# Kernel tuning notes

Hardware: AMD Instinct MI355X
Metric: run time of the kernel (lower is better)

The kernel has to match this reference:

```python
import jax, jax.numpy as jnp
import numpy as np

EPS = 1e-6  # flax nnx LayerNorm default

def _ln(x):
    # LayerNorm without scale/bias
    m = jnp.mean(x, axis=-1, keepdims=True)
    v = jnp.mean(jnp.square(x - m), axis=-1, keepdims=True)
    return (x - m) * jax.lax.rsqrt(v + EPS)

def _modulate(x, shift, scale):
    return x * (1.0 + scale[:, None]) + shift[:, None]

def setup_inputs() -> dict:
    key = jax.random.key(0)
    B, S, H, NH = 8, 1024, 1024, 16
    ks = jax.random.split(key, 12)
    s = lambda k, sh: jax.random.normal(k, sh, dtype=jnp.float32) * 0.02
    return {
        "x": jax.random.normal(ks[0], (B, S, H), dtype=jnp.float32),
        "c": jax.random.normal(ks[1], (B, H), dtype=jnp.float32),
        "w_ada": s(ks[2], (H, 6 * H)),
        "b_ada": jnp.zeros((6 * H,), dtype=jnp.float32),
        "w_qkv": s(ks[3], (H, 3 * H)),
        "w_proj": s(ks[4], (H, H)),
        "b_proj": jnp.zeros((H,), dtype=jnp.float32),
        "w_mlp1": s(ks[5], (H, 4 * H)),
        "b_mlp1": jnp.zeros((4 * H,), dtype=jnp.float32),
        "w_mlp2": s(ks[6], (4 * H, H)),
        "b_mlp2": jnp.zeros((H,), dtype=jnp.float32),
    }

def reference(x, c, w_ada, b_ada, w_qkv, w_proj, b_proj, w_mlp1, b_mlp1, w_mlp2, b_mlp2):
    B, S, H = x.shape
    NH = 16
    CH = H // NH
    # adaLN modulation: silu -> Linear
    cmod = jax.nn.silu(c) @ w_ada + b_ada  # [B, 6H]
    shift_msa, scale_msa, gate_msa, shift_mlp, scale_mlp, gate_mlp = jnp.split(cmod, 6, axis=-1)
    # attention branch
    x_mod = _modulate(_ln(x), shift_msa, scale_msa)
    qkv = x_mod @ w_qkv  # [B, S, 3H]
    k, q, v = jnp.split(qkv, 3, axis=-1)  # note source order: k, q, v
    k = k.reshape(B, S, NH, CH)
    q = q.reshape(B, S, NH, CH)
    v = v.reshape(B, S, NH, CH)
    q = q / CH  # faithful: divide by head_dim (not sqrt)
    w = jnp.einsum('bqhc,bkhc->bhqk', q, k).astype(jnp.float32)
    w = jax.nn.softmax(w, axis=-1)
    y = jnp.einsum('bhqk,bkhc->bqhc', w, v).reshape(B, S, H)
    attn_x = y @ w_proj + b_proj
    x = x + gate_msa[:, None] * attn_x
    # MLP branch
    x_mod2 = _modulate(_ln(x), shift_mlp, scale_mlp)
    h = jax.nn.gelu(x_mod2 @ w_mlp1 + b_mlp1)
    mlp_x = h @ w_mlp2 + b_mlp2
    x = x + gate_mlp[:, None] * mlp_x
    return x
```

## Files before the change

### kernel.cpp

```cpp
#include <hip/hip_runtime.h>
#include <stdint.h>

typedef unsigned short u16;
using bf16x8 = __attribute__((ext_vector_type(8))) __bf16;
using f32x4  = __attribute__((ext_vector_type(4))) float;

#define MFMA16(a,b,c) __builtin_amdgcn_mfma_f32_16x16x32_bf16((a),(b),(c),0,0,0)

__device__ __forceinline__ u16 f2bf(float f) {
  union { float f; uint32_t u; } v; v.f = f;
  uint32_t r = v.u + 0x7FFFu + ((v.u >> 16) & 1u);
  return (u16)(r >> 16);
}

__device__ __forceinline__ void gload_lds16(const void* g, void* l) {
  typedef const __attribute__((address_space(1))) void* gp_t;
  typedef __attribute__((address_space(3))) void* lp_t;
  __builtin_amdgcn_global_load_lds((gp_t)(uintptr_t)g,
                                   (lp_t)(uint32_t)(uintptr_t)l, 16, 0, 0);
}

__global__ __launch_bounds__(256)
void adaln_part_k(const float* __restrict__ c, const float* __restrict__ w,
                  float* __restrict__ partial) {
  const int jb = blockIdx.x, ks = blockIdx.y;
  const int j = jb * 256 + threadIdx.x;
  __shared__ float sil[8][32];
  {
    int b = threadIdx.x >> 5, kk = threadIdx.x & 31;
    float v = c[b * 1024 + ks * 32 + kk];
    sil[b][kk] = v / (1.f + __expf(-v));
  }
  __syncthreads();
  float acc[8] = {0,0,0,0,0,0,0,0};
#pragma unroll 8
  for (int kk = 0; kk < 32; ++kk) {
    float wv = w[(size_t)(ks * 32 + kk) * 6144 + j];
#pragma unroll
    for (int b = 0; b < 8; ++b) acc[b] += sil[b][kk] * wv;
  }
#pragma unroll
  for (int b = 0; b < 8; ++b)
    partial[((size_t)ks * 8 + b) * 6144 + j] = acc[b];
}

__global__ __launch_bounds__(256)
void adaln_red_k(const float* __restrict__ partial, const float* __restrict__ bias,
                 float* __restrict__ cmod) {
  int g = blockIdx.x * 256 + threadIdx.x;
  int j = g % 6144;
  float s = bias[j];
#pragma unroll 8
  for (int ks = 0; ks < 32; ++ks)
    s += partial[(size_t)ks * 8 * 6144 + g];
  cmod[g] = s;
}

__global__ __launch_bounds__(256)
void tcast_k(const float* __restrict__ in, u16* __restrict__ out, int K, int N,
             int lo, int hi, float scale) {
  __shared__ u16 t[64][65];
  int n0 = blockIdx.x * 64, k0 = blockIdx.y * 64;
#pragma unroll
  for (int i = 0; i < 16; ++i) {
    int idx = i * 256 + threadIdx.x;
    int r = idx >> 6, cc = idx & 63;
    float v = in[(size_t)(k0 + r) * N + n0 + cc];
    int n = n0 + cc;
    if (n >= lo && n < hi) v *= scale;
    t[r][cc] = f2bf(v);
  }
  __syncthreads();
#pragma unroll
  for (int i = 0; i < 16; ++i) {
    int idx = i * 256 + threadIdx.x;
    int r = idx >> 6, cc = idx & 63;
    out[(size_t)(n0 + r) * K + k0 + cc] = t[cc][r];
  }
}

__global__ __launch_bounds__(256)
void lnmod_k(const float* __restrict__ x, const float* __restrict__ cmod,
             int shift_off, int scale_off, u16* __restrict__ out) {
  int row = blockIdx.x;
  int b = row >> 10;
  const float4* xr = (const float4*)(x + (size_t)row * 1024);
  float4 v = xr[threadIdx.x];
  float s = v.x + v.y + v.z + v.w;
  float sq = v.x * v.x + v.y * v.y + v.z * v.z + v.w * v.w;
#pragma unroll
  for (int m = 32; m >= 1; m >>= 1) {
    s  += __shfl_xor(s, m);
    sq += __shfl_xor(sq, m);
  }
  __shared__ float ss[4], ssq[4];
  int wave = threadIdx.x >> 6, lane = threadIdx.x & 63;
  if (lane == 0) { ss[wave] = s; ssq[wave] = sq; }
  __syncthreads();
  s  = ss[0] + ss[1] + ss[2] + ss[3];
  sq = ssq[0] + ssq[1] + ssq[2] + ssq[3];
  float mean = s * (1.f / 1024.f);
  float var  = sq * (1.f / 1024.f) - mean * mean;
  float rstd = rsqrtf(var + 1e-6f);
  int col = threadIdx.x * 4;
  const float* sh = cmod + (size_t)b * 6144 + shift_off + col;
  const float* sc = cmod + (size_t)b * 6144 + scale_off + col;
  float xv[4] = {v.x, v.y, v.z, v.w};
  union { u16 o[4]; uint64_t u; } pk;
#pragma unroll
  for (int j = 0; j < 4; ++j)
    pk.o[j] = f2bf((xv[j] - mean) * rstd * (1.f + sc[j]) + sh[j]);
  *(uint64_t*)(out + (size_t)row * 1024 + col) = pk.u;
}

__global__ __launch_bounds__(256)
void tv_k(const u16* __restrict__ qkv, u16* __restrict__ vt) {
  __shared__ u16 t[64][65];
  int r0 = blockIdx.x * 64;
  int h = blockIdx.y;
  int b = r0 >> 10;
  int s0 = r0 & 1023;
#pragma unroll
  for (int i = 0; i < 16; ++i) {
    int idx = i * 256 + threadIdx.x;
    int r = idx >> 6, cc = idx & 63;
    t[r][cc] = qkv[(size_t)(r0 + r) * 3072 + 2048 + h * 64 + cc];
  }
  __syncthreads();
#pragma unroll
  for (int i = 0; i < 16; ++i) {
    int idx = i * 256 + threadIdx.x;
    int ch = idx >> 6, scc = idx & 63;
    vt[((size_t)(b * 16 + h) * 64 + ch) * 1024 + s0 + scc] = t[scc][ch];
  }
}

__device__ __forceinline__ float gelu_f(float x) {
  float z = 1.5957691216057308f * (x + 0.044715f * x * x * x);
  return x / (1.f + __expf(-z));
}

template <int EP>
__global__ __launch_bounds__(512, 2)
void gemm_k(const u16* __restrict__ A, const u16* __restrict__ Bt,
            int N, int K,
            const float* __restrict__ bias, const float* __restrict__ resid,
            const float* __restrict__ gate, void* __restrict__ outp) {
  __shared__ __align__(16) u16 Asb[3][256 * 64];
  __shared__ __align__(16) u16 Bsb[3][128 * 64];
  const int bn = blockIdx.x, bm = blockIdx.y;
  const int tid = threadIdx.x;
  const int wave = tid >> 6, lane = tid & 63;
  const int l15 = lane & 15, lhi = lane >> 4;
  const int wr = wave >> 1, wc = wave & 1;
  const int nkt = K >> 6;
  const size_t arow0 = (size_t)bm * 256;
  const size_t brow0 = (size_t)bn * 128;

  f32x4 acc[4][4] = {};

  auto stage = [&](int buf, int kt) {
    const u16* ab = A  + arow0 * K + (size_t)kt * 64;
    const u16* bb = Bt + brow0 * K + (size_t)kt * 64;
#pragma unroll
    for (int i = 0; i < 4; ++i) {
      int q = i * 512 + tid;
      int r = q >> 3, c = (q & 7) ^ (r & 7);
      gload_lds16(ab + (size_t)r * K + c * 8, &Asb[buf][(i * 8 + wave) * 512]);
    }
#pragma unroll
    for (int i = 0; i < 2; ++i) {
      int q = i * 512 + tid;
      int r = q >> 3, c = (q & 7) ^ (r & 7);
      gload_lds16(bb + (size_t)r * K + c * 8, &Bsb[buf][(i * 8 + wave) * 512]);
    }
  };

  stage(0, 0);
  if (nkt > 1) stage(1, 1);
  asm volatile("s_waitcnt vmcnt(6)" ::: "memory");
  __syncthreads();

  for (int t = 0; t < nkt; ++t) {
    const int s = t % 3;
    if (t + 2 < nkt) stage((t + 2) % 3, t + 2);

    bf16x8 af[4][2], bfr[4][2];
#pragma unroll
    for (int m = 0; m < 4; ++m) {
      int r = wr * 64 + m * 16 + l15;
#pragma unroll
      for (int kh = 0; kh < 2; ++kh) {
        int c = (kh * 4 + lhi) ^ (r & 7);
        af[m][kh] = *(const bf16x8*)&Asb[s][r * 64 + c * 8];
      }
    }
#pragma unroll
    for (int n = 0; n < 4; ++n) {
      int r = wc * 64 + n * 16 + l15;
#pragma unroll
      for (int kh = 0; kh < 2; ++kh) {
        int c = (kh * 4 + lhi) ^ (r & 7);
        bfr[n][kh] = *(const bf16x8*)&Bsb[s][r * 64 + c * 8];
      }
    }
    __builtin_amdgcn_s_setprio(1);
#pragma unroll
    for (int kh = 0; kh < 2; ++kh)
#pragma unroll
      for (int m = 0; m < 4; ++m)
#pragma unroll
        for (int n = 0; n < 4; ++n)
          acc[m][n] = MFMA16(af[m][kh], bfr[n][kh], acc[m][n]);
    __builtin_amdgcn_s_setprio(0);

    if (t + 1 < nkt) {
      if (t + 2 < nkt) asm volatile("s_waitcnt vmcnt(6)" ::: "memory");
      else             asm volatile("s_waitcnt vmcnt(0)" ::: "memory");
      __syncthreads();
    }
  }

#pragma unroll
  for (int m = 0; m < 4; ++m) {
    int row = bm * 256 + wr * 64 + m * 16 + lhi * 4;
#pragma unroll
    for (int n = 0; n < 4; ++n) {
      int col = bn * 128 + wc * 64 + n * 16 + l15;
#pragma unroll
      for (int r = 0; r < 4; ++r) {
        int rr = row + r;
        float v = acc[m][n][r];
        if (EP == 0) {
          ((u16*)outp)[(size_t)rr * N + col] = f2bf(v);
        } else if (EP == 1) {
          ((u16*)outp)[(size_t)rr * N + col] = f2bf(gelu_f(v + bias[col]));
        } else {
          float t2 = v + bias[col];
          int b = rr >> 10;
          float res = resid[(size_t)rr * N + col];
          ((float*)outp)[(size_t)rr * N + col] = res + gate[(size_t)b * 6144 + col] * t2;
        }
      }
    }
  }
}

__global__ __launch_bounds__(256)
void attn_k(const u16* __restrict__ qkv, const u16* __restrict__ vt,
            u16* __restrict__ y) {
  const int qt = blockIdx.x, h = blockIdx.y, b = blockIdx.z;
  const int tid = threadIdx.x, wave = tid >> 6, lane = tid & 63;
  const int l15 = lane & 15, lhi = lane >> 4;
  __shared__ __align__(16) u16 Qs[64 * 64];
  __shared__ __align__(16) u16 Ks[2][64 * 64];
  __shared__ __align__(16) u16 Vs[2][64 * 64];
  __shared__ __align__(16) u16 Ps[64 * 64];
  const size_t qrow0 = (size_t)b * 1024 + qt * 64;
  const size_t krow0 = (size_t)b * 1024;
  const size_t vrow0 = (size_t)(b * 16 + h) * 64;

  auto stageQ = [&]() {
#pragma unroll
    for (int i = 0; i < 2; ++i) {
      int c = (i * 4 + wave) * 64 + lane;
      int r = c >> 3, j = (c & 7) ^ (c >> 3 & 7);
      gload_lds16(qkv + (qrow0 + r) * 3072 + 1024 + h * 64 + j * 8,
                  &Qs[(i * 4 + wave) * 512]);
    }
  };
  auto stageKV = [&](int buf, int kt) {
#pragma unroll
    for (int i = 0; i < 2; ++i) {
      int c = (i * 4 + wave) * 64 + lane;
      int r = c >> 3, j = (c & 7) ^ (c >> 3 & 7);
      gload_lds16(qkv + (krow0 + kt * 64 + r) * 3072 + h * 64 + j * 8,
                  &Ks[buf][(i * 4 + wave) * 512]);
      gload_lds16(vt + (vrow0 + r) * 1024 + kt * 64 + j * 8,
                  &Vs[buf][(i * 4 + wave) * 512]);
    }
  };
  auto ldb = [](const u16* base, int row, int cc) -> bf16x8 {
    return *(const bf16x8*)&base[row * 64 + ((cc ^ (row & 7)) << 3)];
  };

  stageQ();
  stageKV(0, 0);
  __syncthreads();
  bf16x8 qf[2];
  qf[0] = ldb(Qs, wave * 16 + l15, lhi);
  qf[1] = ldb(Qs, wave * 16 + l15, 4 + lhi);

  bf16x8 ones;
#pragma unroll
  for (int j = 0; j < 8; ++j) ones[j] = (__bf16)1.0f;

  float m_r[4];
  f32x4 o[5] = {};
#pragma unroll
  for (int r = 0; r < 4; ++r) m_r[r] = -3.0e38f;

  for (int kt = 0; kt < 16; ++kt) {
    int cur = kt & 1;
    if (kt < 15) stageKV(cur ^ 1, kt + 1);
    f32x4 sf[4] = {};
    __builtin_amdgcn_s_setprio(1);
#pragma unroll
    for (int n = 0; n < 4; ++n) {
      bf16x8 k0 = ldb(Ks[cur], n * 16 + l15, lhi);
      bf16x8 k1 = ldb(Ks[cur], n * 16 + l15, 4 + lhi);
      sf[n] = MFMA16(qf[0], k0, sf[n]);
      sf[n] = MFMA16(qf[1], k1, sf[n]);
    }
    __builtin_amdgcn_s_setprio(0);
#pragma unroll
    for (int r = 0; r < 4; ++r) {
      float mx = fmaxf(fmaxf(sf[0][r], sf[1][r]), fmaxf(sf[2][r], sf[3][r]));
      mx = fmaxf(mx, __shfl_xor(mx, 1));
      mx = fmaxf(mx, __shfl_xor(mx, 2));
      mx = fmaxf(mx, __shfl_xor(mx, 4));
      mx = fmaxf(mx, __shfl_xor(mx, 8));
      float mn = fmaxf(m_r[r], mx);
      float al = __expf(m_r[r] - mn);
      m_r[r] = mn;
      float p0 = __expf(sf[0][r] - mn);
      float p1 = __expf(sf[1][r] - mn);
      float p2 = __expf(sf[2][r] - mn);
      float p3 = __expf(sf[3][r] - mn);
      o[0][r] *= al; o[1][r] *= al; o[2][r] *= al; o[3][r] *= al; o[4][r] *= al;
      int row = wave * 16 + lhi * 4 + r;
      int rb = row * 64, sw = (row & 7) << 3;
      Ps[rb + (l15 ^ sw)]        = f2bf(p0);
      Ps[rb + ((l15 + 16) ^ sw)] = f2bf(p1);
      Ps[rb + ((l15 + 32) ^ sw)] = f2bf(p2);
      Ps[rb + ((l15 + 48) ^ sw)] = f2bf(p3);
    }
    bf16x8 pf0 = ldb(Ps, wave * 16 + l15, lhi);
    bf16x8 pf1 = ldb(Ps, wave * 16 + l15, 4 + lhi);
    __builtin_amdgcn_s_setprio(1);
#pragma unroll
    for (int n = 0; n < 4; ++n) {
      bf16x8 v0 = ldb(Vs[cur], n * 16 + l15, lhi);
      bf16x8 v1 = ldb(Vs[cur], n * 16 + l15, 4 + lhi);
      o[n] = MFMA16(pf0, v0, o[n]);
      o[n] = MFMA16(pf1, v1, o[n]);
    }
    o[4] = MFMA16(pf0, ones, o[4]);
    o[4] = MFMA16(pf1, ones, o[4]);
    __builtin_amdgcn_s_setprio(0);
    __syncthreads();
  }
#pragma unroll
  for (int r = 0; r < 4; ++r) {
    float inv = 1.0f / o[4][r];
    size_t yrow = (qrow0 + wave * 16 + lhi * 4 + r) * 1024 + h * 64 + l15;
    y[yrow]      = f2bf(o[0][r] * inv);
    y[yrow + 16] = f2bf(o[1][r] * inv);
    y[yrow + 32] = f2bf(o[2][r] * inv);
    y[yrow + 48] = f2bf(o[3][r] * inv);
  }
}

extern "C" void kernel_launch(void* const* d_in, const int* in_sizes, int n_in,
                              void* d_out, int out_size, void* d_ws, size_t ws_size,
                              hipStream_t stream) {
  const float* x      = (const float*)d_in[0];
  const float* c      = (const float*)d_in[1];
  const float* w_ada  = (const float*)d_in[2];
  const float* b_ada  = (const float*)d_in[3];
  const float* w_qkv  = (const float*)d_in[4];
  const float* w_proj = (const float*)d_in[5];
  const float* b_proj = (const float*)d_in[6];
  const float* w_mlp1 = (const float*)d_in[7];
  const float* b_mlp1 = (const float*)d_in[8];
  const float* w_mlp2 = (const float*)d_in[9];
  const float* b_mlp2 = (const float*)d_in[10];
  float* out = (float*)d_out;

  char* ws = (char*)d_ws;
  size_t off = 0;
  auto alloc = [&](size_t bytes) {
    void* p = ws + off;
    off += (bytes + 255) & ~(size_t)255;
    return p;
  };
  float* cmod  = (float*)alloc((size_t)8 * 6144 * 4);
  float* apart = (float*)alloc((size_t)32 * 8 * 6144 * 4);
  u16* wqkvT   = (u16*)alloc((size_t)3072 * 1024 * 2);
  u16* wprojT  = (u16*)alloc((size_t)1024 * 1024 * 2);
  u16* wmlp1T  = (u16*)alloc((size_t)4096 * 1024 * 2);
  u16* wmlp2T  = (u16*)alloc((size_t)1024 * 4096 * 2);
  u16* xmod    = (u16*)alloc((size_t)8192 * 1024 * 2);
  u16* qkv     = (u16*)alloc((size_t)8192 * 3072 * 2);
  u16* vt      = (u16*)alloc((size_t)8 * 16 * 64 * 1024 * 2);
  float* x1    = (float*)alloc((size_t)8192 * 1024 * 4);
  u16* hbuf    = (u16*)alloc((size_t)8192 * 4096 * 2);
  u16* ybuf  = xmod;
  u16* xmod2 = qkv;

  adaln_part_k<<<dim3(24, 32), 256, 0, stream>>>(c, w_ada, apart);
  adaln_red_k<<<192, 256, 0, stream>>>(apart, b_ada, cmod);
  tcast_k<<<dim3(3072 / 64, 1024 / 64), 256, 0, stream>>>(w_qkv,  wqkvT,  1024, 3072,
                                                          1024, 2048, 1.0f / 64.0f);
  tcast_k<<<dim3(1024 / 64, 1024 / 64), 256, 0, stream>>>(w_proj, wprojT, 1024, 1024, 0, 0, 1.f);
  tcast_k<<<dim3(4096 / 64, 1024 / 64), 256, 0, stream>>>(w_mlp1, wmlp1T, 1024, 4096, 0, 0, 1.f);
  tcast_k<<<dim3(1024 / 64, 4096 / 64), 256, 0, stream>>>(w_mlp2, wmlp2T, 4096, 1024, 0, 0, 1.f);
  lnmod_k<<<8192, 256, 0, stream>>>(x, cmod, 0, 1024, xmod);
  gemm_k<0><<<dim3(3072 / 128, 8192 / 256), 512, 0, stream>>>(
      xmod, wqkvT, 3072, 1024, nullptr, nullptr, nullptr, qkv);
  tv_k<<<dim3(128, 16), 256, 0, stream>>>(qkv, vt);
  attn_k<<<dim3(16, 16, 8), 256, 0, stream>>>(qkv, vt, ybuf);
  gemm_k<2><<<dim3(1024 / 128, 8192 / 256), 512, 0, stream>>>(
      ybuf, wprojT, 1024, 1024, b_proj, x, cmod + 2048, x1);
  lnmod_k<<<8192, 256, 0, stream>>>(x1, cmod, 3072, 4096, xmod2);
  gemm_k<1><<<dim3(4096 / 128, 8192 / 256), 512, 0, stream>>>(
      xmod2, wmlp1T, 4096, 1024, b_mlp1, nullptr, nullptr, hbuf);
  gemm_k<2><<<dim3(1024 / 128, 8192 / 256), 512, 0, stream>>>(
      hbuf, wmlp2T, 1024, 4096, b_mlp2, x1, cmod + 5120, out);
}
```

Measured before the change: 417.3 us.

## Restructure GEMM into 8-wave ping-pong schedule with interleaved prefetch and barriers

The GEMM kernel changes its wave layout from 4x2 to 2x4 and gives each wave two 64-row halves of A against two 16-column B fragments. Each K-step is split into four MFMA phases separated by s_barrier and sched_barrier, and the next tile's global-to-LDS loads are issued in thirds between the phases. The aim is to overlap LDS fragment loads and global prefetch with MFMA work and keep waves in lockstep. The cost is many more barriers per K-step and a different LDS read pattern, which may stall if phases are unbalanced.

```diff
diff --git a/kernel.cpp b/kernel.cpp
--- a/kernel.cpp
+++ b/kernel.cpp
@@ -6,6 +6,7 @@
 using f32x4  = __attribute__((ext_vector_type(4))) float;
 
 #define MFMA16(a,b,c) __builtin_amdgcn_mfma_f32_16x16x32_bf16((a),(b),(c),0,0,0)
+#define SB0() __builtin_amdgcn_sched_barrier(0)
 
 __device__ __forceinline__ u16 f2bf(float f) {
   union { float f; uint32_t u; } v; v.f = f;
@@ -142,104 +143,144 @@
 
 template <int EP>
 __global__ __launch_bounds__(512, 2)
-void gemm_k(const u16* __restrict__ A, const u16* __restrict__ Bt,
-            int N, int K,
-            const float* __restrict__ bias, const float* __restrict__ resid,
-            const float* __restrict__ gate, void* __restrict__ outp) {
-  __shared__ __align__(16) u16 Asb[3][256 * 64];
-  __shared__ __align__(16) u16 Bsb[3][128 * 64];
+void gemm8_k(const u16* __restrict__ A, const u16* __restrict__ Bt,
+             int N, int K,
+             const float* __restrict__ bias, const float* __restrict__ resid,
+             const float* __restrict__ gate, void* __restrict__ outp) {
+  __shared__ __align__(16) u16 As[3][256 * 64];
+  __shared__ __align__(16) u16 Bs[3][128 * 64];
   const int bn = blockIdx.x, bm = blockIdx.y;
   const int tid = threadIdx.x;
   const int wave = tid >> 6, lane = tid & 63;
   const int l15 = lane & 15, lhi = lane >> 4;
-  const int wr = wave >> 1, wc = wave & 1;
+  const int wm = wave >> 2, wn = wave & 3;
   const int nkt = K >> 6;
   const size_t arow0 = (size_t)bm * 256;
   const size_t brow0 = (size_t)bn * 128;
 
-  f32x4 acc[4][4] = {};
-
-  auto stage = [&](int buf, int kt) {
-    const u16* ab = A  + arow0 * K + (size_t)kt * 64;
-    const u16* bb = Bt + brow0 * K + (size_t)kt * 64;
-#pragma unroll
-    for (int i = 0; i < 4; ++i) {
-      int q = i * 512 + tid;
-      int r = q >> 3, c = (q & 7) ^ (r & 7);
-      gload_lds16(ab + (size_t)r * K + c * 8, &Asb[buf][(i * 8 + wave) * 512]);
-    }
-#pragma unroll
-    for (int i = 0; i < 2; ++i) {
-      int q = i * 512 + tid;
-      int r = q >> 3, c = (q & 7) ^ (r & 7);
-      gload_lds16(bb + (size_t)r * K + c * 8, &Bsb[buf][(i * 8 + wave) * 512]);
-    }
-  };
-
-  stage(0, 0);
-  if (nkt > 1) stage(1, 1);
-  asm volatile("s_waitcnt vmcnt(6)" ::: "memory");
-  __syncthreads();
-
-  for (int t = 0; t < nkt; ++t) {
-    const int s = t % 3;
-    if (t + 2 < nkt) stage((t + 2) % 3, t + 2);
-
-    bf16x8 af[4][2], bfr[4][2];
+  f32x4 acc[2][4][2] = {};
+
+  auto stage_half = [&](int half, int w, int kt) {
+    if (half < 2) {
+      const u16* ab = A + (arow0 + half * 128) * (size_t)K + (size_t)kt * 64;
+#pragma unroll
+      for (int i = 0; i < 2; ++i) {
+        int q = i * 512 + tid;
+        int r = q >> 3, cc = (q & 7) ^ (r & 7);
+        gload_lds16(ab + (size_t)r * K + cc * 8,
+                    &As[w][(half * 16 + i * 8 + wave) * 512]);
+      }
+    } else {
+      const u16* bb = Bt + brow0 * (size_t)K + (size_t)kt * 64;
+#pragma unroll
+      for (int i = 0; i < 2; ++i) {
+        int q = i * 512 + tid;
+        int r = q >> 3, cc = (q & 7) ^ (r & 7);
+        gload_lds16(bb + (size_t)r * K + cc * 8,
+                    &Bs[w][(i * 8 + wave) * 512]);
+      }
+    }
+  };
+  auto lda = [&](int s, int mh, int m, int kk) -> bf16x8 {
+    int r = wm * 128 + mh * 64 + m * 16 + l15;
+    int cc = (kk * 4 + lhi) ^ (r & 7);
+    return *(const bf16x8*)&As[s][r * 64 + cc * 8];
+  };
+  auto ldbf = [&](int s, int nh, int kk) -> bf16x8 {
+    int r = wn * 32 + nh * 16 + l15;
+    int cc = (kk * 4 + lhi) ^ (r & 7);
+    return *(const bf16x8*)&Bs[s][r * 64 + cc * 8];
+  };
+
+  stage_half(0, 0, 0); stage_half(1, 0, 0); stage_half(2, 0, 0);
+  if (nkt > 1) {
+    stage_half(0, 1, 1); stage_half(1, 1, 1); stage_half(2, 1, 1);
+    asm volatile("s_waitcnt vmcnt(6)" ::: "memory");
+  } else {
+    asm volatile("s_waitcnt vmcnt(0)" ::: "memory");
+  }
+  SB0(); __builtin_amdgcn_s_barrier(); SB0();
+
+  for (int kt = 0; kt < nkt; ++kt) {
+    const int s = kt % 3, w2 = (kt + 2) % 3;
+    const bool pf = (kt + 2 < nkt);
+    bf16x8 afr[4][2], bfr[2][2];
+
+#pragma unroll
+    for (int m = 0; m < 4; ++m) { afr[m][0] = lda(s, 0, m, 0); afr[m][1] = lda(s, 0, m, 1); }
+    bfr[0][0] = ldbf(s, 0, 0); bfr[0][1] = ldbf(s, 0, 1);
+    if (pf) stage_half(0, w2, kt + 2);
+    SB0(); __builtin_amdgcn_s_barrier(); SB0();
+    __builtin_amdgcn_s_setprio(1);
 #pragma unroll
     for (int m = 0; m < 4; ++m) {
-      int r = wr * 64 + m * 16 + l15;
-#pragma unroll
-      for (int kh = 0; kh < 2; ++kh) {
-        int c = (kh * 4 + lhi) ^ (r & 7);
-        af[m][kh] = *(const bf16x8*)&Asb[s][r * 64 + c * 8];
-      }
-    }
-#pragma unroll
-    for (int n = 0; n < 4; ++n) {
-      int r = wc * 64 + n * 16 + l15;
-#pragma unroll
-      for (int kh = 0; kh < 2; ++kh) {
-        int c = (kh * 4 + lhi) ^ (r & 7);
-        bfr[n][kh] = *(const bf16x8*)&Bsb[s][r * 64 + c * 8];
-      }
-    }
-    __builtin_amdgcn_s_setprio(1);
-#pragma unroll
-    for (int kh = 0; kh < 2; ++kh)
-#pragma unroll
-      for (int m = 0; m < 4; ++m)
-#pragma unroll
-        for (int n = 0; n < 4; ++n)
-          acc[m][n] = MFMA16(af[m][kh], bfr[n][kh], acc[m][n]);
-    __builtin_amdgcn_s_setprio(0);
-
-    if (t + 1 < nkt) {
-      if (t + 2 < nkt) asm volatile("s_waitcnt vmcnt(6)" ::: "memory");
-      else             asm volatile("s_waitcnt vmcnt(0)" ::: "memory");
-      __syncthreads();
-    }
-  }
-
-#pragma unroll
-  for (int m = 0; m < 4; ++m) {
-    int row = bm * 256 + wr * 64 + m * 16 + lhi * 4;
-#pragma unroll
-    for (int n = 0; n < 4; ++n) {
-      int col = bn * 128 + wc * 64 + n * 16 + l15;
-#pragma unroll
-      for (int r = 0; r < 4; ++r) {
-        int rr = row + r;
-        float v = acc[m][n][r];
-        if (EP == 0) {
-          ((u16*)outp)[(size_t)rr * N + col] = f2bf(v);
-        } else if (EP == 1) {
-          ((u16*)outp)[(size_t)rr * N + col] = f2bf(gelu_f(v + bias[col]));
-        } else {
-          float t2 = v + bias[col];
-          int b = rr >> 10;
-          float res = resid[(size_t)rr * N + col];
-          ((float*)outp)[(size_t)rr * N + col] = res + gate[(size_t)b * 6144 + col] * t2;
+      acc[0][m][0] = MFMA16(afr[m][0], bfr[0][0], acc[0][m][0]);
+      acc[0][m][0] = MFMA16(afr[m][1], bfr[0][1], acc[0][m][0]);
+    }
+    __builtin_amdgcn_s_setprio(0);
+    SB0(); __builtin_amdgcn_s_barrier(); SB0();
+
+    bfr[1][0] = ldbf(s, 1, 0); bfr[1][1] = ldbf(s, 1, 1);
+    if (pf) stage_half(1, w2, kt + 2);
+    SB0(); __builtin_amdgcn_s_barrier(); SB0();
+    __builtin_amdgcn_s_setprio(1);
+#pragma unroll
+    for (int m = 0; m < 4; ++m) {
+      acc[0][m][1] = MFMA16(afr[m][0], bfr[1][0], acc[0][m][1]);
+      acc[0][m][1] = MFMA16(afr[m][1], bfr[1][1], acc[0][m][1]);
+    }
+    __builtin_amdgcn_s_setprio(0);
+    SB0(); __builtin_amdgcn_s_barrier(); SB0();
+
+#pragma unroll
+    for (int m = 0; m < 4; ++m) { afr[m][0] = lda(s, 1, m, 0); afr[m][1] = lda(s, 1, m, 1); }
+    if (pf) stage_half(2, w2, kt + 2);
+    SB0(); __builtin_amdgcn_s_barrier(); SB0();
+    __builtin_amdgcn_s_setprio(1);
+#pragma unroll
+    for (int m = 0; m < 4; ++m) {
+      acc[1][m][0] = MFMA16(afr[m][0], bfr[0][0], acc[1][m][0]);
+      acc[1][m][0] = MFMA16(afr[m][1], bfr[0][1], acc[1][m][0]);
+    }
+    __builtin_amdgcn_s_setprio(0);
+    SB0(); __builtin_amdgcn_s_barrier(); SB0();
+
+    __builtin_amdgcn_s_setprio(1);
+#pragma unroll
+    for (int m = 0; m < 4; ++m) {
+      acc[1][m][1] = MFMA16(afr[m][0], bfr[1][0], acc[1][m][1]);
+      acc[1][m][1] = MFMA16(afr[m][1], bfr[1][1], acc[1][m][1]);
+    }
+    __builtin_amdgcn_s_setprio(0);
+    if (kt + 1 < nkt) {
+      if (pf) asm volatile("s_waitcnt vmcnt(6)" ::: "memory");
+      else    asm volatile("s_waitcnt vmcnt(0)" ::: "memory");
+      SB0(); __builtin_amdgcn_s_barrier(); SB0();
+    }
+  }
+
+#pragma unroll
+  for (int mh = 0; mh < 2; ++mh) {
+#pragma unroll
+    for (int m = 0; m < 4; ++m) {
+      int row = bm * 256 + wm * 128 + mh * 64 + m * 16 + lhi * 4;
+#pragma unroll
+      for (int nh = 0; nh < 2; ++nh) {
+        int col = bn * 128 + wn * 32 + nh * 16 + l15;
+#pragma unroll
+        for (int r = 0; r < 4; ++r) {
+          int rr = row + r;
+          float v = acc[mh][m][nh][r];
+          if (EP == 0) {
+            ((u16*)outp)[(size_t)rr * N + col] = f2bf(v);
+          } else if (EP == 1) {
+            ((u16*)outp)[(size_t)rr * N + col] = f2bf(gelu_f(v + bias[col]));
+          } else {
+            float t2 = v + bias[col];
+            int b = rr >> 10;
+            float res = resid[(size_t)rr * N + col];
+            ((float*)outp)[(size_t)rr * N + col] = res + gate[(size_t)b * 6144 + col] * t2;
+          }
         }
       }
     }
@@ -406,15 +447,15 @@
   tcast_k<<<dim3(4096 / 64, 1024 / 64), 256, 0, stream>>>(w_mlp1, wmlp1T, 1024, 4096, 0, 0, 1.f);
   tcast_k<<<dim3(1024 / 64, 4096 / 64), 256, 0, stream>>>(w_mlp2, wmlp2T, 4096, 1024, 0, 0, 1.f);
   lnmod_k<<<8192, 256, 0, stream>>>(x, cmod, 0, 1024, xmod);
-  gemm_k<0><<<dim3(3072 / 128, 8192 / 256), 512, 0, stream>>>(
+  gemm8_k<0><<<dim3(3072 / 128, 8192 / 256), 512, 0, stream>>>(
       xmod, wqkvT, 3072, 1024, nullptr, nullptr, nullptr, qkv);
   tv_k<<<dim3(128, 16), 256, 0, stream>>>(qkv, vt);
   attn_k<<<dim3(16, 16, 8), 256, 0, stream>>>(qkv, vt, ybuf);
-  gemm_k<2><<<dim3(1024 / 128, 8192 / 256), 512, 0, stream>>>(
+  gemm8_k<2><<<dim3(1024 / 128, 8192 / 256), 512, 0, stream>>>(
       ybuf, wprojT, 1024, 1024, b_proj, x, cmod + 2048, x1);
   lnmod_k<<<8192, 256, 0, stream>>>(x1, cmod, 3072, 4096, xmod2);
-  gemm_k<1><<<dim3(4096 / 128, 8192 / 256), 512, 0, stream>>>(
+  gemm8_k<1><<<dim3(4096 / 128, 8192 / 256), 512, 0, stream>>>(
       xmod2, wmlp1T, 4096, 1024, b_mlp1, nullptr, nullptr, hbuf);
-  gemm_k<2><<<dim3(1024 / 128, 8192 / 256), 512, 0, stream>>>(
+  gemm8_k<2><<<dim3(1024 / 128, 8192 / 256), 512, 0, stream>>>(
       hbuf, wmlp2T, 1024, 4096, b_mlp2, x1, cmod + 5120, out);
 }
```

New measurement: 433.0 us. 1.04x slower.

## Use 256x256 GEMM tiles with phased 8-wave MFMA/prefetch interleave

Applied to the files above, without the earlier changes.

Replaces the 256x128 triple-buffered GEMM with a 256x256 tile, double buffered, where 8 waves each compute 128x64 in four phases separated by barriers. Next-tile loads are interleaved between MFMA phases once a buffer half is consumed. The larger tile raises arithmetic intensity and reduces redundant global loads. The risks are halved grid sizes, notably 128 blocks for the N=1024 GEMMs, more barriers, and higher LDS use limiting occupancy.

```diff
diff --git a/kernel.cpp b/kernel.cpp
--- a/kernel.cpp
+++ b/kernel.cpp
@@ -142,91 +142,144 @@
 
 template <int EP>
 __global__ __launch_bounds__(512, 2)
-void gemm_k(const u16* __restrict__ A, const u16* __restrict__ Bt,
-            int N, int K,
-            const float* __restrict__ bias, const float* __restrict__ resid,
-            const float* __restrict__ gate, void* __restrict__ outp) {
-  __shared__ __align__(16) u16 Asb[3][256 * 64];
-  __shared__ __align__(16) u16 Bsb[3][128 * 64];
+void gemm8_k(const u16* __restrict__ A, const u16* __restrict__ Bt,
+             int N, int K,
+             const float* __restrict__ bias, const float* __restrict__ resid,
+             const float* __restrict__ gate, void* __restrict__ outp) {
+  __shared__ __align__(16) u16 As[2][256 * 64];
+  __shared__ __align__(16) u16 Bs[2][256 * 64];
   const int bn = blockIdx.x, bm = blockIdx.y;
   const int tid = threadIdx.x;
   const int wave = tid >> 6, lane = tid & 63;
   const int l15 = lane & 15, lhi = lane >> 4;
-  const int wr = wave >> 1, wc = wave & 1;
+  const int wm = wave >> 2, wn = wave & 3;
   const int nkt = K >> 6;
   const size_t arow0 = (size_t)bm * 256;
-  const size_t brow0 = (size_t)bn * 128;
-
-  f32x4 acc[4][4] = {};
-
-  auto stage = [&](int buf, int kt) {
-    const u16* ab = A  + arow0 * K + (size_t)kt * 64;
-    const u16* bb = Bt + brow0 * K + (size_t)kt * 64;
-#pragma unroll
-    for (int i = 0; i < 4; ++i) {
-      int q = i * 512 + tid;
-      int r = q >> 3, c = (q & 7) ^ (r & 7);
-      gload_lds16(ab + (size_t)r * K + c * 8, &Asb[buf][(i * 8 + wave) * 512]);
-    }
+  const size_t brow0 = (size_t)bn * 256;
+
+  f32x4 acc[8][4] = {};
+
+  auto stage_half = [&](const u16* mat, size_t row0, u16* dst, int kt) {
+    const u16* src = mat + row0 * K + (size_t)kt * 64;
 #pragma unroll
     for (int i = 0; i < 2; ++i) {
       int q = i * 512 + tid;
-      int r = q >> 3, c = (q & 7) ^ (r & 7);
-      gload_lds16(bb + (size_t)r * K + c * 8, &Bsb[buf][(i * 8 + wave) * 512]);
-    }
-  };
-
-  stage(0, 0);
-  if (nkt > 1) stage(1, 1);
-  asm volatile("s_waitcnt vmcnt(6)" ::: "memory");
-  __syncthreads();
-
-  for (int t = 0; t < nkt; ++t) {
-    const int s = t % 3;
-    if (t + 2 < nkt) stage((t + 2) % 3, t + 2);
-
-    bf16x8 af[4][2], bfr[4][2];
+      int r = q >> 3, cc = (q & 7) ^ (r & 7);
+      gload_lds16(src + (size_t)r * K + cc * 8, dst + (i * 8 + wave) * 512);
+    }
+  };
+  auto lda = [&](int cur, int row, int kh) -> bf16x8 {
+    int cc = (kh * 4 + lhi) ^ (row & 7);
+    return *(const bf16x8*)&As[cur][row * 64 + cc * 8];
+  };
+  auto ldb = [&](int cur, int row, int kh) -> bf16x8 {
+    int cc = (kh * 4 + lhi) ^ (row & 7);
+    return *(const bf16x8*)&Bs[cur][row * 64 + cc * 8];
+  };
+
+  stage_half(A, arow0,       &As[0][0],        0);
+  stage_half(A, arow0 + 128, &As[0][128 * 64], 0);
+  stage_half(Bt, brow0,       &Bs[0][0],        0);
+  stage_half(Bt, brow0 + 128, &Bs[0][128 * 64], 0);
+  stage_half(A, arow0,       &As[1][0],        1);
+  stage_half(A, arow0 + 128, &As[1][128 * 64], 1);
+  stage_half(Bt, brow0,       &Bs[1][0],        1);
+  stage_half(Bt, brow0 + 128, &Bs[1][128 * 64], 1);
+  asm volatile("s_waitcnt vmcnt(8)" ::: "memory");
+  __builtin_amdgcn_s_barrier();
+
+  bf16x8 afr[4][2], bfr[4][2];
+  for (int kt = 0; kt < nkt; ++kt) {
+    const int cur = kt & 1;
+    const bool pf = (kt + 2 < nkt);
+
 #pragma unroll
     for (int m = 0; m < 4; ++m) {
-      int r = wr * 64 + m * 16 + l15;
-#pragma unroll
-      for (int kh = 0; kh < 2; ++kh) {
-        int c = (kh * 4 + lhi) ^ (r & 7);
-        af[m][kh] = *(const bf16x8*)&Asb[s][r * 64 + c * 8];
+      int r = wm * 128 + m * 16 + l15;
+      afr[m][0] = lda(cur, r, 0); afr[m][1] = lda(cur, r, 1);
+    }
+#pragma unroll
+    for (int n = 0; n < 2; ++n) {
+      int r = wn * 64 + n * 16 + l15;
+      bfr[n][0] = ldb(cur, r, 0); bfr[n][1] = ldb(cur, r, 1);
+    }
+    __builtin_amdgcn_s_barrier();
+    __builtin_amdgcn_s_setprio(1);
+#pragma unroll
+    for (int m = 0; m < 4; ++m)
+#pragma unroll
+      for (int n = 0; n < 2; ++n) {
+        acc[m][n] = MFMA16(afr[m][0], bfr[n][0], acc[m][n]);
+        acc[m][n] = MFMA16(afr[m][1], bfr[n][1], acc[m][n]);
       }
-    }
+    __builtin_amdgcn_s_setprio(0);
+    __builtin_amdgcn_s_barrier();
+
+#pragma unroll
+    for (int n = 2; n < 4; ++n) {
+      int r = wn * 64 + n * 16 + l15;
+      bfr[n][0] = ldb(cur, r, 0); bfr[n][1] = ldb(cur, r, 1);
+    }
+    __builtin_amdgcn_s_barrier();
+    __builtin_amdgcn_s_setprio(1);
+#pragma unroll
+    for (int m = 0; m < 4; ++m)
+#pragma unroll
+      for (int n = 2; n < 4; ++n) {
+        acc[m][n] = MFMA16(afr[m][0], bfr[n][0], acc[m][n]);
+        acc[m][n] = MFMA16(afr[m][1], bfr[n][1], acc[m][n]);
+      }
+    __builtin_amdgcn_s_setprio(0);
+    __builtin_amdgcn_s_barrier();
+
+#pragma unroll
+    for (int m = 0; m < 4; ++m) {
+      int r = wm * 128 + 64 + m * 16 + l15;
+      afr[m][0] = lda(cur, r, 0); afr[m][1] = lda(cur, r, 1);
+    }
+    if (pf) {
+      stage_half(Bt, brow0,       &Bs[cur][0],        kt + 2);
+      stage_half(Bt, brow0 + 128, &Bs[cur][128 * 64], kt + 2);
+    }
+    __builtin_amdgcn_s_barrier();
+    __builtin_amdgcn_s_setprio(1);
+#pragma unroll
+    for (int m = 0; m < 4; ++m)
+#pragma unroll
+      for (int n = 0; n < 2; ++n) {
+        acc[m + 4][n] = MFMA16(afr[m][0], bfr[n][0], acc[m + 4][n]);
+        acc[m + 4][n] = MFMA16(afr[m][1], bfr[n][1], acc[m + 4][n]);
+      }
+    __builtin_amdgcn_s_setprio(0);
+    __builtin_amdgcn_s_barrier();
+
+    if (pf) {
+      stage_half(A, arow0,       &As[cur][0],        kt + 2);
+      stage_half(A, arow0 + 128, &As[cur][128 * 64], kt + 2);
+    }
+    __builtin_amdgcn_s_barrier();
+    __builtin_amdgcn_s_setprio(1);
+#pragma unroll
+    for (int m = 0; m < 4; ++m)
+#pragma unroll
+      for (int n = 2; n < 4; ++n) {
+        acc[m + 4][n] = MFMA16(afr[m][0], bfr[n][0], acc[m + 4][n]);
+        acc[m + 4][n] = MFMA16(afr[m][1], bfr[n][1], acc[m + 4][n]);
+      }
+    __builtin_amdgcn_s_setprio(0);
+    if (kt + 1 < nkt) {
+      if (pf) asm volatile("s_waitcnt vmcnt(8)" ::: "memory");
+      else    asm volatile("s_waitcnt vmcnt(0)" ::: "memory");
+      __builtin_amdgcn_s_barrier();
+    }
+  }
+
+#pragma unroll
+  for (int m = 0; m < 8; ++m) {
+    int row = bm * 256 + wm * 128 + m * 16 + lhi * 4;
 #pragma unroll
     for (int n = 0; n < 4; ++n) {
-      int r = wc * 64 + n * 16 + l15;
-#pragma unroll
-      for (int kh = 0; kh < 2; ++kh) {
-        int c = (kh * 4 + lhi) ^ (r & 7);
-        bfr[n][kh] = *(const bf16x8*)&Bsb[s][r * 64 + c * 8];
-      }
-    }
-    __builtin_amdgcn_s_setprio(1);
-#pragma unroll
-    for (int kh = 0; kh < 2; ++kh)
-#pragma unroll
-      for (int m = 0; m < 4; ++m)
-#pragma unroll
-        for (int n = 0; n < 4; ++n)
-          acc[m][n] = MFMA16(af[m][kh], bfr[n][kh], acc[m][n]);
-    __builtin_amdgcn_s_setprio(0);
-
-    if (t + 1 < nkt) {
-      if (t + 2 < nkt) asm volatile("s_waitcnt vmcnt(6)" ::: "memory");
-      else             asm volatile("s_waitcnt vmcnt(0)" ::: "memory");
-      __syncthreads();
-    }
-  }
-
-#pragma unroll
-  for (int m = 0; m < 4; ++m) {
-    int row = bm * 256 + wr * 64 + m * 16 + lhi * 4;
-#pragma unroll
-    for (int n = 0; n < 4; ++n) {
-      int col = bn * 128 + wc * 64 + n * 16 + l15;
+      int col = bn * 256 + wn * 64 + n * 16 + l15;
 #pragma unroll
       for (int r = 0; r < 4; ++r) {
         int rr = row + r;
@@ -406,15 +459,15 @@
   tcast_k<<<dim3(4096 / 64, 1024 / 64), 256, 0, stream>>>(w_mlp1, wmlp1T, 1024, 4096, 0, 0, 1.f);
   tcast_k<<<dim3(1024 / 64, 4096 / 64), 256, 0, stream>>>(w_mlp2, wmlp2T, 4096, 1024, 0, 0, 1.f);
   lnmod_k<<<8192, 256, 0, stream>>>(x, cmod, 0, 1024, xmod);
-  gemm_k<0><<<dim3(3072 / 128, 8192 / 256), 512, 0, stream>>>(
+  gemm8_k<0><<<dim3(3072 / 256, 8192 / 256), 512, 0, stream>>>(
       xmod, wqkvT, 3072, 1024, nullptr, nullptr, nullptr, qkv);
   tv_k<<<dim3(128, 16), 256, 0, stream>>>(qkv, vt);
   attn_k<<<dim3(16, 16, 8), 256, 0, stream>>>(qkv, vt, ybuf);
-  gemm_k<2><<<dim3(1024 / 128, 8192 / 256), 512, 0, stream>>>(
+  gemm8_k<2><<<dim3(1024 / 256, 8192 / 256), 512, 0, stream>>>(
       ybuf, wprojT, 1024, 1024, b_proj, x, cmod + 2048, x1);
   lnmod_k<<<8192, 256, 0, stream>>>(x1, cmod, 3072, 4096, xmod2);
-  gemm_k<1><<<dim3(4096 / 128, 8192 / 256), 512, 0, stream>>>(
+  gemm8_k<1><<<dim3(4096 / 256, 8192 / 256), 512, 0, stream>>>(
       xmod2, wmlp1T, 4096, 1024, b_mlp1, nullptr, nullptr, hbuf);
-  gemm_k<2><<<dim3(1024 / 128, 8192 / 256), 512, 0, stream>>>(
+  gemm8_k<2><<<dim3(1024 / 256, 8192 / 256), 512, 0, stream>>>(
       hbuf, wmlp2T, 1024, 4096, b_mlp2, x1, cmod + 5120, out);
 }
```

Measured after the change: 459.1 us. 1.1x slower.
